# Performance work log

Hardware: AMD Instinct MI355X
Metric: run time of the kernel (lower is better)

The kernel has to match this reference:

```python
import jax, jax.numpy as jnp
import numpy as np
from jax import lax

INPUT_DIM = 512
OUTPUT_DIM = 256
MAX_HIDDEN = 1024
NUM_NODES = INPUT_DIM + OUTPUT_DIM + MAX_HIDDEN      # 1792
NUM_MID = OUTPUT_DIM + MAX_HIDDEN                    # 1280
BATCH = 16384


def setup_inputs() -> dict:
    key = jax.random.key(0)
    k1, k2, k3, k4, k5 = jax.random.split(key, 5)
    x = jax.random.normal(k1, (BATCH, INPUT_DIM), dtype=jnp.float32)
    weight = jax.random.normal(k2, (NUM_NODES, NUM_MID), dtype=jnp.float32) * 0.1
    bias = jax.random.normal(k3, (NUM_MID,), dtype=jnp.float32) * 0.1
    connectivity = jax.random.randint(k4, (NUM_NODES, NUM_MID), 0, 2, dtype=jnp.int32)
    node_existence = jax.random.randint(k5, (NUM_MID,), 0, 2, dtype=jnp.int32)
    node_existence = node_existence.at[-OUTPUT_DIM:].set(1)  # outputs always exist
    return {"x": x, "weight": weight, "bias": bias,
            "connectivity": connectivity, "node_existence": node_existence}


def reference(x, weight, bias, connectivity, node_existence):
    B = x.shape[0]
    eff_w = weight * connectivity.astype(weight.dtype)        # [N, M]
    exist = node_existence.astype(x.dtype)                    # [M]
    # results buffer [B, N]; slots >= INPUT_DIM+i are zero before step i,
    # so a full-length dot equals the torch sliced dot results[:, :input_dim+i] @ w[:input_dim+i, i].
    results = jnp.zeros((B, NUM_NODES), dtype=x.dtype).at[:, :INPUT_DIM].set(x)

    def step(results, inputs):
        i, w_col, b, e = inputs
        res = (jax.nn.sigmoid(results @ w_col) + b) * e       # [B]  (bias added AFTER sigmoid, as in torch)
        return results.at[:, INPUT_DIM + i].set(res), None

    results, _ = lax.scan(
        step, results,
        (jnp.arange(NUM_MID), eff_w.T, bias, exist))
    return results[:, -OUTPUT_DIM:]
```

## Files before the change

### kernel.cpp

```cpp
#include <hip/hip_runtime.h>

#define IN_DIM   512
#define OUT_DIM  256
#define N_MID    1280
#define BATCH    16384
#define NT       256
#define XPAD     520


#define EW2_ELEMS ((size_t)48 * 64 * 64 * 8)
#define EW2_BYTES (EW2_ELEMS * 2)
#define TRI_OFF   EW2_BYTES
#define TRI_BYTES ((size_t)32 * 1024 * 4)
#define HDR_OFF   (TRI_OFF + TRI_BYTES)
#define CMAP_OFF  (HDR_OFF + 32)
#define OCOL_OFF  (CMAP_OFF + N_MID * 4)
#define BIASC_OFF (OCOL_OFF + N_MID * 4)
#define BFX_OFF   (BIASC_OFF + N_MID * 4)
#define BFX_BYTES ((size_t)32 * 64 * 8 * 2)
#define WS_NEED   (BFX_OFF + BFX_BYTES)

#define NEG_LOG2E (-1.44269504088896340736f)

typedef __attribute__((ext_vector_type(8))) short  bfrag;
typedef __attribute__((ext_vector_type(4))) float  ffrag;

__device__ __forceinline__ unsigned short f2bf(float f) {
    unsigned int u = __float_as_uint(f);
    u += 0x7FFFu + ((u >> 16) & 1u);
    return (unsigned short)(u >> 16);
}

__device__ __forceinline__ float fast_exp2(float x) {
#if __has_builtin(__builtin_amdgcn_exp2f)
    return __builtin_amdgcn_exp2f(x);
#else
    float r;
    asm("v_exp_f32 %0, %1" : "=v"(r) : "v"(x));
    return r;
#endif
}

__device__ __forceinline__ float fast_rcp(float x) {
#if __has_builtin(__builtin_amdgcn_rcpf)
    return __builtin_amdgcn_rcpf(x);
#else
    float r;
    asm("v_rcp_f32 %0, %1" : "=v"(r) : "v"(x));
    return r;
#endif
}

__device__ __forceinline__ unsigned int cvt_pk_bf16(float lo, float hi) {
    unsigned int r;
    asm("v_cvt_pk_bf16_f32 %0, %1, %2" : "=v"(r) : "v"(lo), "v"(hi));
    return r;
}

__global__ void build_maps_kernel(const int* __restrict__ exist,
                                  const float* __restrict__ bias,
                                  int* __restrict__ hdr,
                                  int* __restrict__ cmap,
                                  int* __restrict__ ocol,
                                  float* __restrict__ biasc) {
    const int lane = threadIdx.x;
    int base = 0;
    for (int r = 0; r < N_MID / 64; ++r) {
        const int i = r * 64 + lane;
        const int e = exist[i];
        const unsigned long long m  = __ballot(e != 0);
        const unsigned long long lt = (lane == 0) ? 0ull : (~0ull >> (64 - lane));
        const int pos = base + __popcll(m & lt);
        if (e) {
            cmap[pos]  = i;
            ocol[pos]  = (i >= N_MID - OUT_DIM) ? (i - (N_MID - OUT_DIM)) : -1;
            biasc[pos] = bias[i];
        }
        base += __popcll(m);
    }
    for (int idx = base + lane; idx < N_MID; idx += 64) {
        cmap[idx] = 0; ocol[idx] = -1; biasc[idx] = 0.f;
    }
    if (lane == 0) {
        const int Mc = base;
        int Mpad;
        if (Mc <= 768) Mpad = 768;
        else if (Mc <= 1024) Mpad = 1024;
        else Mpad = (Mc + 127) & ~127;
        hdr[0] = Mc; hdr[1] = Mpad; hdr[2] = 0;
        hdr[3] = Mpad / 32; hdr[4] = Mpad / 16;
    }
}

__global__ __launch_bounds__(NT)
void gather_all_kernel(const float* __restrict__ w, const int* __restrict__ conn,
                       const int* __restrict__ hdr, const int* __restrict__ cmap,
                       unsigned short* __restrict__ ew2, float* __restrict__ tri,
                       unsigned short* __restrict__ bfx) {
    const int Mc = hdr[0], nch = hdr[3], tpm = hdr[4];
    const int bx = blockIdx.x;
    if (bx < 768) {
        if (tpm > 64) return;
        const int tid  = bx * NT + threadIdx.x;
        const int lane = tid & 63;
        const int gl   = tid >> 6;
        const int gt   = gl % tpm;
        const int kstep = gl / tpm;
        if (kstep >= 16 + nch) return;
        const int c  = gt * 16 + (lane & 15);
        const int k0 = kstep * 32 + ((lane >> 4) << 3);
        unsigned short v[8];
#pragma unroll
        for (int jj = 0; jj < 8; ++jj) {
            const int s = k0 + jj;
            float val = 0.f;
            if (c < Mc) {
                const int cc = cmap[c];
                if (s < IN_DIM) {
                    const size_t o = (size_t)s * N_MID + cc;
                    val = w[o] * (float)conn[o] * NEG_LOG2E;
                } else {
                    const int s2 = s - IN_DIM;
                    if (s2 < Mc && s2 < c && (s2 >> 5) != (c >> 5)) {
                        const size_t o = (size_t)(IN_DIM + cmap[s2]) * N_MID + cc;
                        val = w[o] * (float)conn[o] * NEG_LOG2E;
                    }
                }
            }
            v[jj] = f2bf(val);
        }
        *(uint4*)&ew2[((size_t)(kstep * tpm + gt) * 64 + lane) * 8] = *(uint4*)v;
    } else if (bx < 896) {
        if (tpm > 64) return;
        const int idx = (bx - 768) * NT + threadIdx.x;
        const int j  = idx >> 10;
        if (j >= nch) return;
        const int sl = (idx >> 5) & 31;
        const int cl = idx & 31;
        const int s = j * 32 + sl, c = j * 32 + cl;
        float v = 0.f;
        if (sl < cl && c < Mc) {
            const size_t o = (size_t)(IN_DIM + cmap[s]) * N_MID + cmap[c];
            v = w[o] * (float)conn[o] * NEG_LOG2E;
        }
        tri[idx] = v;
    } else {
        if (tpm > 64) return;
        const int j = (bx - 896) * 4 + (threadIdx.x >> 6);
        if (j >= nch || j >= 32) return;
        const int lane = threadIdx.x & 63;
        const int cl = lane & 15, qq = lane >> 4;
        const int cg = 32 * j + 16 + cl;
        unsigned short v[8];
#pragma unroll
        for (int jj = 0; jj < 8; ++jj) {
            const int k = qq * 8 + jj;
            float val = 0.f;
            if (k < 16 && cg < Mc) {
                const size_t o = (size_t)(IN_DIM + cmap[32 * j + k]) * N_MID + cmap[cg];
                val = w[o] * (float)conn[o] * NEG_LOG2E;
            }
            v[jj] = f2bf(val);
        }
        *(uint4*)&bfx[((size_t)j * 64 + lane) * 8] = *(uint4*)v;
    }
}

__device__ __forceinline__ float f4c(const float4& v, int k) {
    return (k == 0) ? v.x : (k == 1) ? v.y : (k == 2) ? v.z : v.w;
}

template <int TPW>
__global__ __launch_bounds__(256)
__attribute__((amdgpu_waves_per_eu(1, 1)))
void net7_kernel(const float* __restrict__ x,
                 const unsigned short* __restrict__ ew2,
                 const float* __restrict__ tri_g,
                 const int* __restrict__ hdr,
                 const int* __restrict__ ocol,
                 const float* __restrict__ biasc,
                 const unsigned short* __restrict__ bfx,
                 float* __restrict__ out) {
    if (hdr[1] != TPW * 64) return;
    const int Mc  = hdr[0];
    const int tpm = TPW * 4;
    const int nch = TPW * 2;

    __shared__ __align__(16) unsigned short xa[4096 * 8];
    __shared__ __align__(16) float stage2[32 * 68];
    __shared__ __align__(16) unsigned short res2[2][2048];
    __shared__ __align__(16) float tri_lds[2][1024];
    __shared__ float bias_lds[1024];
    __shared__ int   ocol_lds[1024];

    const int t = threadIdx.x, lane = t & 63, w = t >> 6;
    const int l15 = lane & 15, q = lane >> 4;
    const int r0 = blockIdx.x * 64;
    const int g0 = w * TPW;

    for (int i = t; i < TPW * 64; i += 256) {
        bias_lds[i] = biasc[i];
        ocol_lds[i] = ocol[i];
    }
    {
        uint4 z; z.x = 0u; z.y = 0u; z.z = 0u; z.w = 0u;
        uint4* r2 = (uint4*)res2;
        for (int i = t; i < 512; i += 256) r2[i] = z;
    }
    if (w == 3) {
        const float4* src = (const float4*)tri_g;
#pragma unroll
        for (int u = 0; u < 4; ++u)
            *(float4*)&tri_lds[0][(lane + 64 * u) * 4] = src[lane + 64 * u];
    }
    for (int i = t; i < 4096; i += 256) {
        const int lane2 = i & 63, rrkb = i >> 6;
        const int rr = rrkb & 3, kb = rrkb >> 2;
        const int qq = lane2 >> 4, ll = lane2 & 15;
        const int row = rr * 16 + ll;
        const int k0 = kb * 32 + qq * 8;
        const float4 f0 = *(const float4*)&x[(size_t)(r0 + row) * IN_DIM + k0];
        const float4 f1 = *(const float4*)&x[(size_t)(r0 + row) * IN_DIM + k0 + 4];
        unsigned int uu[4] = {cvt_pk_bf16(f0.x, f0.y), cvt_pk_bf16(f0.z, f0.w),
                              cvt_pk_bf16(f1.x, f1.y), cvt_pk_bf16(f1.z, f1.w)};
        *(uint4*)&xa[(size_t)i * 8] = *(uint4*)uu;
    }
    __syncthreads();

    ffrag acc[TPW][4];
#pragma unroll
    for (int tt = 0; tt < TPW; ++tt)
#pragma unroll
        for (int rr = 0; rr < 4; ++rr) acc[tt][rr] = (ffrag)0.f;

#pragma unroll 1
    for (int kb = 0; kb < 16; ++kb) {
        bfrag a[4];
#pragma unroll
        for (int rr = 0; rr < 4; ++rr)
            a[rr] = *(const bfrag*)&xa[((kb * 4 + rr) * 64 + lane) * 8];
#pragma unroll
        for (int tt = 0; tt < TPW; ++tt) {
            if ((g0 + tt) * 16 < Mc) {
                const bfrag b = *(const bfrag*)&ew2[((size_t)(kb * tpm + g0 + tt) * 64 + lane) * 8];
#pragma unroll
                for (int rr = 0; rr < 4; ++rr)
                    acc[tt][rr] = __builtin_amdgcn_mfma_f32_16x16x32_bf16(a[rr], b, acc[tt][rr], 0, 0, 0);
            }
        }
    }

    bfrag bpre[TPW];
#pragma unroll 1
    for (int j = 0; j < nch; ++j) {
        const int cbase = 32 * j;
        if (cbase >= Mc) break;

        const bfrag bc = *(const bfrag*)&bfx[((size_t)j * 64 + lane) * 8];

        if (j > 0) {
            const int pr = (j - 1) & 1;
            bfrag a[4];
#pragma unroll
            for (int rr = 0; rr < 4; ++rr)
                a[rr] = *(const bfrag*)&res2[pr][(rr * 64 + lane) * 8];
#pragma unroll
            for (int tt = 0; tt < TPW; ++tt) {
                const int col0 = (g0 + tt) * 16;
                if (col0 >= cbase && col0 < Mc) {
#pragma unroll
                    for (int rr = 0; rr < 4; ++rr)
                        acc[tt][rr] = __builtin_amdgcn_mfma_f32_16x16x32_bf16(a[rr], bpre[tt], acc[tt][rr], 0, 0, 0);
                }
            }
        }
#pragma unroll
        for (int tt = 0; tt < TPW; ++tt) {
            const int col0 = (g0 + tt) * 16;
            if (col0 >= 32 * (j + 1) && col0 < Mc)
                bpre[tt] = *(const bfrag*)&ew2[((size_t)((16 + j) * tpm + g0 + tt) * 64 + lane) * 8];
        }

        const int ow = (2 * j) / TPW;
        if (w == ow) {
#pragma unroll
            for (int tt = 0; tt < TPW; ++tt) {
                if (g0 + tt == 2 * j) {
#pragma unroll
                    for (int rr = 0; rr < 4; ++rr)
                        *(ffrag*)&stage2[l15 * 68 + rr * 16 + 4 * q] = acc[tt][rr];
                }
            }
            const float* trij = tri_lds[j & 1];
            float reg[32];
#pragma unroll
            for (int c = 0; c < 16; ++c) reg[c] = stage2[c * 68 + lane];

            float4 tr[2][8];
#pragma unroll
            for (int u = 0; u < 4; ++u) tr[0][u] = *(const float4*)&trij[u * 4];

#pragma unroll
            for (int c = 0; c < 16; ++c) {
                const int cb = c & 1;
                if (c < 15) {
#pragma unroll
                    for (int u = (c + 2) >> 2; u < 4; ++u)
                        tr[cb ^ 1][u] = *(const float4*)&trij[(c + 1) * 32 + u * 4];
                }
                const float e  = fast_exp2(reg[c]);
                const float s  = fast_rcp(1.f + e);
                const float rs = s + bias_lds[cbase + c];
                reg[c] = rs;
#pragma unroll
                for (int k = c + 1; k < 16; ++k)
                    reg[k] = fmaf(rs, f4c(tr[cb][k >> 2], k & 3), reg[k]);
            }
            unsigned short* resb = res2[j & 1];
            const int rowA = (q * 64 + l15) * 8;
#pragma unroll
            for (int qA = 0; qA < 2; ++qA) {
                unsigned int u[4];
#pragma unroll
                for (int i = 0; i < 4; ++i)
                    u[i] = cvt_pk_bf16(reg[qA * 8 + 2 * i], reg[qA * 8 + 2 * i + 1]);
                *(uint4*)&resb[rowA + qA * 128] = *(uint4*)u;
            }
            bfrag aB[4];
#pragma unroll
            for (int rr = 0; rr < 4; ++rr)
                aB[rr] = *(const bfrag*)&resb[(rr * 64 + lane) * 8];
#pragma unroll
            for (int tt = 0; tt < TPW; ++tt) {
                if (g0 + tt == 2 * j + 1) {
#pragma unroll
                    for (int rr = 0; rr < 4; ++rr)
                        acc[tt][rr] = __builtin_amdgcn_mfma_f32_16x16x32_bf16(aB[rr], bc, acc[tt][rr], 0, 0, 0);
#pragma unroll
                    for (int rr = 0; rr < 4; ++rr)
                        *(ffrag*)&stage2[(16 + l15) * 68 + rr * 16 + 4 * q] = acc[tt][rr];
                }
            }
#pragma unroll
            for (int c = 16; c < 32; ++c) reg[c] = stage2[c * 68 + lane];
#pragma unroll
            for (int u = 4; u < 8; ++u) tr[0][u] = *(const float4*)&trij[16 * 32 + u * 4];

#pragma unroll
            for (int c = 16; c < 32; ++c) {
                const int cb = c & 1;
                if (c < 31) {
#pragma unroll
                    for (int u = (c + 2) >> 2; u < 8; ++u)
                        tr[cb ^ 1][u] = *(const float4*)&trij[(c + 1) * 32 + u * 4];
                }
                const float e  = fast_exp2(reg[c]);
                const float s  = fast_rcp(1.f + e);
                const float rs = s + bias_lds[cbase + c];
                reg[c] = rs;
#pragma unroll
                for (int k = c + 1; k < 32; ++k)
                    reg[k] = fmaf(rs, f4c(tr[cb][k >> 2], k & 3), reg[k]);
            }
#pragma unroll
            for (int qA = 2; qA < 4; ++qA) {
                unsigned int u[4];
#pragma unroll
                for (int i = 0; i < 4; ++i)
                    u[i] = cvt_pk_bf16(reg[qA * 8 + 2 * i], reg[qA * 8 + 2 * i + 1]);
                *(uint4*)&resb[rowA + qA * 128] = *(uint4*)u;
            }
#pragma unroll
            for (int c4 = 0; c4 < 8; ++c4) {
                const int oc0 = ocol_lds[cbase + c4 * 4];
                const int oc3 = ocol_lds[cbase + c4 * 4 + 3];
                if (oc0 >= 0 && oc3 == oc0 + 3 && (oc0 & 3) == 0) {
                    const float4 v = make_float4(reg[c4 * 4], reg[c4 * 4 + 1],
                                                 reg[c4 * 4 + 2], reg[c4 * 4 + 3]);
                    *(float4*)&out[(size_t)(r0 + lane) * OUT_DIM + oc0] = v;
                } else {
#pragma unroll
                    for (int c = c4 * 4; c < c4 * 4 + 4; ++c) {
                        const int oc = ocol_lds[cbase + c];
                        if (oc >= 0)
                            out[(size_t)(r0 + lane) * OUT_DIM + oc] = reg[c];
                    }
                }
            }
        } else if (w == ((ow + 2) & 3)) {
            const int jn = j + 1;
            if (jn < nch && 32 * jn < Mc) {
                const float4* src = (const float4*)(tri_g + (size_t)jn * 1024);
#pragma unroll
                for (int u = 0; u < 4; ++u)
                    *(float4*)&tri_lds[jn & 1][(lane + 64 * u) * 4] = src[lane + 64 * u];
            }
        }
        __syncthreads();
    }
}

__global__ __launch_bounds__(NT, 4)
void net_v1_kernel(const float* __restrict__ x,
                   const float* __restrict__ wsrc,
                   const int* __restrict__ conn,
                   const float* __restrict__ bias,
                   const int* __restrict__ exist,
                   const int* __restrict__ hdr,
                   float* __restrict__ out) {
    if (hdr && hdr[1] <= 1024) return;
    __shared__ float xs[16 * XPAD];
    __shared__ float res_s[2][16];
    float* bias_s  = xs;
    float* exist_s = xs + N_MID;
    const int t = threadIdx.x, rg = t & 3, cg = t >> 2;
    const int r0 = blockIdx.x * 16;
    const int c0 = cg * 20;
    {
        const float4* xg = (const float4*)(x + (size_t)r0 * IN_DIM);
        for (int idx = t; idx < 16 * IN_DIM / 4; idx += NT) {
            const int r = idx >> 7, jj = idx & 127;
            *(float4*)&xs[r * XPAD + jj * 4] = xg[idx];
        }
    }
    __syncthreads();
    float acc[4][20];
#pragma unroll
    for (int a = 0; a < 4; ++a)
#pragma unroll
        for (int k = 0; k < 20; ++k) acc[a][k] = 0.f;
    for (int j = 0; j < IN_DIM; ++j) {
        const size_t woff = (size_t)j * N_MID + c0;
        const float xv0 = xs[rg * XPAD + j];
        const float xv1 = xs[(rg + 4) * XPAD + j];
        const float xv2 = xs[(rg + 8) * XPAD + j];
        const float xv3 = xs[(rg + 12) * XPAD + j];
#pragma unroll
        for (int qq = 0; qq < 5; ++qq) {
            float4 w4 = *(const float4*)(wsrc + woff + qq * 4);
            const int4 c4 = *(const int4*)(conn + woff + qq * 4);
            w4.x *= (float)c4.x; w4.y *= (float)c4.y;
            w4.z *= (float)c4.z; w4.w *= (float)c4.w;
            const float wq[4] = {w4.x, w4.y, w4.z, w4.w};
#pragma unroll
            for (int u = 0; u < 4; ++u) {
                const int k = qq * 4 + u;
                acc[0][k] = fmaf(xv0, wq[u], acc[0][k]);
                acc[1][k] = fmaf(xv1, wq[u], acc[1][k]);
                acc[2][k] = fmaf(xv2, wq[u], acc[2][k]);
                acc[3][k] = fmaf(xv3, wq[u], acc[3][k]);
            }
        }
    }
    __syncthreads();
    for (int idx = t; idx < N_MID; idx += NT) {
        bias_s[idx]  = bias[idx];
        exist_s[idx] = (float)exist[idx];
    }
    __syncthreads();
    int p = 0;
    for (int bb = 0; bb < 64; ++bb) {
#pragma unroll
        for (int kk = 0; kk < 20; ++kk) {
            const int i = bb * 20 + kk;
            const float e = exist_s[i];
            if (e != 0.f) {
                if (cg == bb) {
                    const float bv = bias_s[i];
#pragma unroll
                    for (int a = 0; a < 4; ++a) {
                        const float v = acc[a][kk];
                        const float s = __fdividef(1.f, 1.f + __expf(-v));
                        const float res = (s + bv) * e;
                        res_s[p][rg + 4 * a] = res;
                        if (i >= N_MID - OUT_DIM)
                            out[(size_t)(r0 + rg + 4 * a) * OUT_DIM + (i - (N_MID - OUT_DIM))] = res;
                    }
                }
                __syncthreads();
                const float rv0 = res_s[p][rg];
                const float rv1 = res_s[p][rg + 4];
                const float rv2 = res_s[p][rg + 8];
                const float rv3 = res_s[p][rg + 12];
                const size_t woff = (size_t)(IN_DIM + i) * N_MID + c0;
                if (cg > bb) {
#pragma unroll
                    for (int qq = 0; qq < 5; ++qq) {
                        float4 w4 = *(const float4*)(wsrc + woff + qq * 4);
                        const int4 c4 = *(const int4*)(conn + woff + qq * 4);
                        w4.x *= (float)c4.x; w4.y *= (float)c4.y;
                        w4.z *= (float)c4.z; w4.w *= (float)c4.w;
                        const float wq[4] = {w4.x, w4.y, w4.z, w4.w};
#pragma unroll
                        for (int u = 0; u < 4; ++u) {
                            const int k = qq * 4 + u;
                            acc[0][k] = fmaf(rv0, wq[u], acc[0][k]);
                            acc[1][k] = fmaf(rv1, wq[u], acc[1][k]);
                            acc[2][k] = fmaf(rv2, wq[u], acc[2][k]);
                            acc[3][k] = fmaf(rv3, wq[u], acc[3][k]);
                        }
                    }
                } else if (cg == bb) {
#pragma unroll
                    for (int k = kk + 1; k < 20; ++k) {
                        float ww = wsrc[woff + k] * (float)conn[woff + k];
                        acc[0][k] = fmaf(rv0, ww, acc[0][k]);
                        acc[1][k] = fmaf(rv1, ww, acc[1][k]);
                        acc[2][k] = fmaf(rv2, ww, acc[2][k]);
                        acc[3][k] = fmaf(rv3, ww, acc[3][k]);
                    }
                }
                p ^= 1;
            }
        }
    }
}

extern "C" void kernel_launch(void* const* d_in, const int* in_sizes, int n_in,
                              void* d_out, int out_size, void* d_ws, size_t ws_size,
                              hipStream_t stream) {
    const float* x      = (const float*)d_in[0];
    const float* weight = (const float*)d_in[1];
    const float* bias   = (const float*)d_in[2];
    const int*   conn   = (const int*)d_in[3];
    const int*   exist  = (const int*)d_in[4];
    float*       out    = (float*)d_out;

    if (ws_size >= WS_NEED) {
        char* ws = (char*)d_ws;
        unsigned short* ew2  = (unsigned short*)ws;
        float*          tri  = (float*)(ws + TRI_OFF);
        int*            hdr  = (int*)(ws + HDR_OFF);
        int*            cmap = (int*)(ws + CMAP_OFF);
        int*            ocolp= (int*)(ws + OCOL_OFF);
        float*          bsc  = (float*)(ws + BIASC_OFF);
        unsigned short* bfx  = (unsigned short*)(ws + BFX_OFF);

        build_maps_kernel<<<1, 64, 0, stream>>>(exist, bias, hdr, cmap, ocolp, bsc);
        gather_all_kernel<<<904, NT, 0, stream>>>(weight, conn, hdr, cmap, ew2, tri, bfx);
        net7_kernel<12><<<256, 256, 0, stream>>>(x, ew2, tri, hdr, ocolp, bsc, bfx, out);
        net7_kernel<16><<<256, 256, 0, stream>>>(x, ew2, tri, hdr, ocolp, bsc, bfx, out);
        net_v1_kernel<<<BATCH / 16, NT, 0, stream>>>(x, weight, conn, bias, exist, hdr, out);
    } else {
        net_v1_kernel<<<BATCH / 16, NT, 0, stream>>>(x, weight, conn, bias, exist, nullptr, out);
    }
}
```

Before: 285.1 us.

## Fold bias into precomputed column offsets and deepen triangular weight prefetch

Precomputes, per compacted column, the weighted sum of all earlier biases (cb) in a new gather branch. The serial sigmoid recurrence can then carry plain sigmoid values, with bias added only when writing outputs. This removes a dependent bias add from each step of the critical chain. The triangular weight loads also move to a 4-deep register prefetch ring instead of the previous 2-slot ping-pong. In exchange, the new cb branch runs a serial loop of up to ~1K strided global loads per thread, which may lengthen the gather kernel. Rounding also shifts slightly because bf16 now stores values without the bias.

After: 519.3 us. 82.1% more time.

```diff
diff --git a/kernel.cpp b/kernel.cpp
--- a/kernel.cpp
+++ b/kernel.cpp
@@ -18,7 +18,9 @@
 #define BIASC_OFF (OCOL_OFF + N_MID * 4)
 #define BFX_OFF   (BIASC_OFF + N_MID * 4)
 #define BFX_BYTES ((size_t)32 * 64 * 8 * 2)
-#define WS_NEED   (BFX_OFF + BFX_BYTES)
+#define CB_OFF    (BFX_OFF + BFX_BYTES)
+#define CB_BYTES  (1024 * 4)
+#define WS_NEED   (CB_OFF + CB_BYTES)
 
 #define NEG_LOG2E (-1.44269504088896340736f)
 
@@ -95,8 +97,9 @@
 __global__ __launch_bounds__(NT)
 void gather_all_kernel(const float* __restrict__ w, const int* __restrict__ conn,
                        const int* __restrict__ hdr, const int* __restrict__ cmap,
+                       const float* __restrict__ biasc,
                        unsigned short* __restrict__ ew2, float* __restrict__ tri,
-                       unsigned short* __restrict__ bfx) {
+                       unsigned short* __restrict__ bfx, float* __restrict__ cb) {
     const int Mc = hdr[0], nch = hdr[3], tpm = hdr[4];
     const int bx = blockIdx.x;
     if (bx < 768) {
@@ -144,7 +147,7 @@
             v = w[o] * (float)conn[o] * NEG_LOG2E;
         }
         tri[idx] = v;
-    } else {
+    } else if (bx < 904) {
         if (tpm > 64) return;
         const int j = (bx - 896) * 4 + (threadIdx.x >> 6);
         if (j >= nch || j >= 32) return;
@@ -163,6 +166,18 @@
             v[jj] = f2bf(val);
         }
         *(uint4*)&bfx[((size_t)j * 64 + lane) * 8] = *(uint4*)v;
+    } else {
+        if (tpm > 64) return;
+        const int k = (bx - 904) * NT + threadIdx.x;
+        float acc = 0.f;
+        if (k < Mc) {
+            const int ck = cmap[k];
+            for (int c = 0; c < k; ++c) {
+                const size_t o = (size_t)(IN_DIM + cmap[c]) * N_MID + ck;
+                acc += w[o] * (float)conn[o] * biasc[c];
+            }
+        }
+        cb[k] = acc * NEG_LOG2E;
     }
 }
 
@@ -180,6 +195,7 @@
                  const int* __restrict__ ocol,
                  const float* __restrict__ biasc,
                  const unsigned short* __restrict__ bfx,
+                 const float* __restrict__ cbg,
                  float* __restrict__ out) {
     if (hdr[1] != TPW * 64) return;
     const int Mc  = hdr[0];
@@ -191,6 +207,7 @@
     __shared__ __align__(16) unsigned short res2[2][2048];
     __shared__ __align__(16) float tri_lds[2][1024];
     __shared__ float bias_lds[1024];
+    __shared__ float cb_lds[1024];
     __shared__ int   ocol_lds[1024];
 
     const int t = threadIdx.x, lane = t & 63, w = t >> 6;
@@ -200,6 +217,7 @@
 
     for (int i = t; i < TPW * 64; i += 256) {
         bias_lds[i] = biasc[i];
+        cb_lds[i]   = cbg[i];
         ocol_lds[i] = ocol[i];
     }
     {
@@ -292,29 +310,33 @@
                 }
             }
             const float* trij = tri_lds[j & 1];
+
+            float4 tr[4][4];
+#pragma unroll
+            for (int r = 0; r < 4; ++r)
+#pragma unroll
+                for (int u = (r + 1) >> 2; u < 4; ++u)
+                    tr[r & 3][u] = *(const float4*)&trij[r * 32 + u * 4];
+
             float reg[32];
 #pragma unroll
-            for (int c = 0; c < 16; ++c) reg[c] = stage2[c * 68 + lane];
-
-            float4 tr[2][8];
-#pragma unroll
-            for (int u = 0; u < 4; ++u) tr[0][u] = *(const float4*)&trij[u * 4];
+            for (int c = 0; c < 16; ++c)
+                reg[c] = stage2[c * 68 + lane] + cb_lds[cbase + c];
 
 #pragma unroll
             for (int c = 0; c < 16; ++c) {
-                const int cb = c & 1;
-                if (c < 15) {
-#pragma unroll
-                    for (int u = (c + 2) >> 2; u < 4; ++u)
-                        tr[cb ^ 1][u] = *(const float4*)&trij[(c + 1) * 32 + u * 4];
-                }
-                const float e  = fast_exp2(reg[c]);
-                const float s  = fast_rcp(1.f + e);
-                const float rs = s + bias_lds[cbase + c];
-                reg[c] = rs;
+                const float e = fast_exp2(reg[c]);
+                const float s = fast_rcp(1.f + e);
+                reg[c] = s;
 #pragma unroll
                 for (int k = c + 1; k < 16; ++k)
-                    reg[k] = fmaf(rs, f4c(tr[cb][k >> 2], k & 3), reg[k]);
+                    reg[k] = fmaf(s, f4c(tr[c & 3][k >> 2], k & 3), reg[k]);
+                const int pf = c + 4;
+                if (pf < 15) {
+#pragma unroll
+                    for (int u = (pf + 1) >> 2; u < 4; ++u)
+                        tr[pf & 3][u] = *(const float4*)&trij[pf * 32 + u * 4];
+                }
             }
             unsigned short* resb = res2[j & 1];
             const int rowA = (q * 64 + l15) * 8;
@@ -326,6 +348,12 @@
                     u[i] = cvt_pk_bf16(reg[qA * 8 + 2 * i], reg[qA * 8 + 2 * i + 1]);
                 *(uint4*)&resb[rowA + qA * 128] = *(uint4*)u;
             }
+#pragma unroll
+            for (int r = 16; r < 20; ++r)
+#pragma unroll
+                for (int u = (r + 1) >> 2; u < 8; ++u)
+                    tr[r & 3][u - 4] = *(const float4*)&trij[r * 32 + u * 4];
+
             bfrag aB[4];
 #pragma unroll
             for (int rr = 0; rr < 4; ++rr)
@@ -342,25 +370,23 @@
                 }
             }
 #pragma unroll
-            for (int c = 16; c < 32; ++c) reg[c] = stage2[c * 68 + lane];
-#pragma unroll
-            for (int u = 4; u < 8; ++u) tr[0][u] = *(const float4*)&trij[16 * 32 + u * 4];
+            for (int c = 16; c < 32; ++c)
+                reg[c] = stage2[c * 68 + lane] + cb_lds[cbase + c];
 
 #pragma unroll
             for (int c = 16; c < 32; ++c) {
-                const int cb = c & 1;
-                if (c < 31) {
-#pragma unroll
-                    for (int u = (c + 2) >> 2; u < 8; ++u)
-                        tr[cb ^ 1][u] = *(const float4*)&trij[(c + 1) * 32 + u * 4];
-                }
-                const float e  = fast_exp2(reg[c]);
-                const float s  = fast_rcp(1.f + e);
-                const float rs = s + bias_lds[cbase + c];
-                reg[c] = rs;
+                const float e = fast_exp2(reg[c]);
+                const float s = fast_rcp(1.f + e);
+                reg[c] = s;
 #pragma unroll
                 for (int k = c + 1; k < 32; ++k)
-                    reg[k] = fmaf(rs, f4c(tr[cb][k >> 2], k & 3), reg[k]);
+                    reg[k] = fmaf(s, f4c(tr[c & 3][(k >> 2) - 4], k & 3), reg[k]);
+                const int pf = c + 4;
+                if (pf < 31) {
+#pragma unroll
+                    for (int u = (pf + 1) >> 2; u < 8; ++u)
+                        tr[pf & 3][u - 4] = *(const float4*)&trij[pf * 32 + u * 4];
+                }
             }
 #pragma unroll
             for (int qA = 2; qA < 4; ++qA) {
@@ -375,15 +401,19 @@
                 const int oc0 = ocol_lds[cbase + c4 * 4];
                 const int oc3 = ocol_lds[cbase + c4 * 4 + 3];
                 if (oc0 >= 0 && oc3 == oc0 + 3 && (oc0 & 3) == 0) {
-                    const float4 v = make_float4(reg[c4 * 4], reg[c4 * 4 + 1],
-                                                 reg[c4 * 4 + 2], reg[c4 * 4 + 3]);
+                    const float4 v = make_float4(
+                        reg[c4 * 4]     + bias_lds[cbase + c4 * 4],
+                        reg[c4 * 4 + 1] + bias_lds[cbase + c4 * 4 + 1],
+                        reg[c4 * 4 + 2] + bias_lds[cbase + c4 * 4 + 2],
+                        reg[c4 * 4 + 3] + bias_lds[cbase + c4 * 4 + 3]);
                     *(float4*)&out[(size_t)(r0 + lane) * OUT_DIM + oc0] = v;
                 } else {
 #pragma unroll
                     for (int c = c4 * 4; c < c4 * 4 + 4; ++c) {
                         const int oc = ocol_lds[cbase + c];
                         if (oc >= 0)
-                            out[(size_t)(r0 + lane) * OUT_DIM + oc] = reg[c];
+                            out[(size_t)(r0 + lane) * OUT_DIM + oc] =
+                                reg[c] + bias_lds[cbase + c];
                     }
                 }
             }
@@ -535,11 +565,13 @@
         int*            ocolp= (int*)(ws + OCOL_OFF);
         float*          bsc  = (float*)(ws + BIASC_OFF);
         unsigned short* bfx  = (unsigned short*)(ws + BFX_OFF);
+        float*          cb   = (float*)(ws + CB_OFF);
 
         build_maps_kernel<<<1, 64, 0, stream>>>(exist, bias, hdr, cmap, ocolp, bsc);
-        gather_all_kernel<<<904, NT, 0, stream>>>(weight, conn, hdr, cmap, ew2, tri, bfx);
-        net7_kernel<12><<<256, 256, 0, stream>>>(x, ew2, tri, hdr, ocolp, bsc, bfx, out);
-        net7_kernel<16><<<256, 256, 0, stream>>>(x, ew2, tri, hdr, ocolp, bsc, bfx, out);
+        gather_all_kernel<<<908, NT, 0, stream>>>(weight, conn, hdr, cmap, bsc,
+                                                  ew2, tri, bfx, cb);
+        net7_kernel<12><<<256, 256, 0, stream>>>(x, ew2, tri, hdr, ocolp, bsc, bfx, cb, out);
+        net7_kernel<16><<<256, 256, 0, stream>>>(x, ew2, tri, hdr, ocolp, bsc, bfx, cb, out);
         net_v1_kernel<<<BATCH / 16, NT, 0, stream>>>(x, weight, conn, bias, exist, hdr, out);
     } else {
         net_v1_kernel<<<BATCH / 16, NT, 0, stream>>>(x, weight, conn, bias, exist, nullptr, out);
```

## Give each wave its own 16 batch rows to remove block-wide barriers

Applied to the files above, without the earlier changes.

Rework the work split inside a block. Each of the four waves now owns 16 batch rows and all output column tiles, where before the waves split column tiles and all shared 64 rows. The serial triangular sigmoid chain therefore runs in every wave at once on its own rows, and the per-chunk __syncthreads is gone. Triangle tiles are now prefetched per wave from global into registers and then into a per-wave LDS double buffer. The cost is more B-fragment global loads per wave, since every wave reads all weight tiles, and lanes 16-63 sit idle during the packing and output steps.

Measured after the change: 615.7 us. +116.0%, slower.

```diff
diff --git a/kernel.cpp b/kernel.cpp
--- a/kernel.cpp
+++ b/kernel.cpp
@@ -173,7 +173,7 @@
 template <int TPW>
 __global__ __launch_bounds__(256)
 __attribute__((amdgpu_waves_per_eu(1, 1)))
-void net7_kernel(const float* __restrict__ x,
+void net9_kernel(const float* __restrict__ x,
                  const unsigned short* __restrict__ ew2,
                  const float* __restrict__ tri_g,
                  const int* __restrict__ hdr,
@@ -182,21 +182,21 @@
                  const unsigned short* __restrict__ bfx,
                  float* __restrict__ out) {
     if (hdr[1] != TPW * 64) return;
+    constexpr int TPM = TPW * 4;
     const int Mc  = hdr[0];
-    const int tpm = TPW * 4;
+    const int tpm = TPM;
     const int nch = TPW * 2;
 
     __shared__ __align__(16) unsigned short xa[4096 * 8];
-    __shared__ __align__(16) float stage2[32 * 68];
-    __shared__ __align__(16) unsigned short res2[2][2048];
-    __shared__ __align__(16) float tri_lds[2][1024];
+    __shared__ __align__(16) float trib_s[4][2][1024];
+    __shared__ __align__(16) float stage_s[4][32 * 20];
+    __shared__ __align__(16) unsigned short apack_s[4][512];
     __shared__ float bias_lds[1024];
     __shared__ int   ocol_lds[1024];
 
     const int t = threadIdx.x, lane = t & 63, w = t >> 6;
     const int l15 = lane & 15, q = lane >> 4;
     const int r0 = blockIdx.x * 64;
-    const int g0 = w * TPW;
 
     for (int i = t; i < TPW * 64; i += 256) {
         bias_lds[i] = biasc[i];
@@ -204,14 +204,12 @@
     }
     {
         uint4 z; z.x = 0u; z.y = 0u; z.z = 0u; z.w = 0u;
-        uint4* r2 = (uint4*)res2;
-        for (int i = t; i < 512; i += 256) r2[i] = z;
-    }
-    if (w == 3) {
-        const float4* src = (const float4*)tri_g;
-#pragma unroll
-        for (int u = 0; u < 4; ++u)
-            *(float4*)&tri_lds[0][(lane + 64 * u) * 4] = src[lane + 64 * u];
+        *(uint4*)&apack_s[w][lane * 8] = z;
+#pragma unroll
+        for (int u = 0; u < 4; ++u) {
+            const float4 tv = *(const float4*)&tri_g[u * 256 + lane * 4];
+            *(float4*)&trib_s[w][0][u * 256 + lane * 4] = tv;
+        }
     }
     for (int i = t; i < 4096; i += 256) {
         const int lane2 = i & 63, rrkb = i >> 6;
@@ -227,149 +225,132 @@
     }
     __syncthreads();
 
-    ffrag acc[TPW][4];
-#pragma unroll
-    for (int tt = 0; tt < TPW; ++tt)
-#pragma unroll
-        for (int rr = 0; rr < 4; ++rr) acc[tt][rr] = (ffrag)0.f;
+    ffrag acc[TPM];
+#pragma unroll
+    for (int tt = 0; tt < TPM; ++tt) acc[tt] = (ffrag)0.f;
 
 #pragma unroll 1
     for (int kb = 0; kb < 16; ++kb) {
-        bfrag a[4];
-#pragma unroll
-        for (int rr = 0; rr < 4; ++rr)
-            a[rr] = *(const bfrag*)&xa[((kb * 4 + rr) * 64 + lane) * 8];
-#pragma unroll
-        for (int tt = 0; tt < TPW; ++tt) {
-            if ((g0 + tt) * 16 < Mc) {
-                const bfrag b = *(const bfrag*)&ew2[((size_t)(kb * tpm + g0 + tt) * 64 + lane) * 8];
-#pragma unroll
-                for (int rr = 0; rr < 4; ++rr)
-                    acc[tt][rr] = __builtin_amdgcn_mfma_f32_16x16x32_bf16(a[rr], b, acc[tt][rr], 0, 0, 0);
-            }
-        }
-    }
-
-    bfrag bpre[TPW];
+        const bfrag a = *(const bfrag*)&xa[((kb * 4 + w) * 64 + lane) * 8];
+#pragma unroll
+        for (int tt = 0; tt < TPM; ++tt) {
+            if (tt * 16 < Mc) {
+                const bfrag b = *(const bfrag*)&ew2[((size_t)(kb * tpm + tt) * 64 + lane) * 8];
+                acc[tt] = __builtin_amdgcn_mfma_f32_16x16x32_bf16(a, b, acc[tt], 0, 0, 0);
+            }
+        }
+    }
+
+    float* stg = stage_s[w];
+    unsigned short* apk = apack_s[w];
+    const int wrow0 = r0 + 16 * w;
+
 #pragma unroll 1
     for (int j = 0; j < nch; ++j) {
         const int cbase = 32 * j;
         if (cbase >= Mc) break;
 
+        const bool tok = (j + 1 < nch) && (32 * (j + 1) < Mc);
+        float4 tpre[4];
+        if (tok) {
+#pragma unroll
+            for (int u = 0; u < 4; ++u)
+                tpre[u] = *(const float4*)&tri_g[(size_t)(j + 1) * 1024 + u * 256 + lane * 4];
+        }
         const bfrag bc = *(const bfrag*)&bfx[((size_t)j * 64 + lane) * 8];
 
-        if (j > 0) {
-            const int pr = (j - 1) & 1;
-            bfrag a[4];
-#pragma unroll
-            for (int rr = 0; rr < 4; ++rr)
-                a[rr] = *(const bfrag*)&res2[pr][(rr * 64 + lane) * 8];
-#pragma unroll
-            for (int tt = 0; tt < TPW; ++tt) {
-                const int col0 = (g0 + tt) * 16;
-                if (col0 >= cbase && col0 < Mc) {
-#pragma unroll
-                    for (int rr = 0; rr < 4; ++rr)
-                        acc[tt][rr] = __builtin_amdgcn_mfma_f32_16x16x32_bf16(a[rr], bpre[tt], acc[tt][rr], 0, 0, 0);
-                }
-            }
-        }
-#pragma unroll
-        for (int tt = 0; tt < TPW; ++tt) {
-            const int col0 = (g0 + tt) * 16;
-            if (col0 >= 32 * (j + 1) && col0 < Mc)
-                bpre[tt] = *(const bfrag*)&ew2[((size_t)((16 + j) * tpm + g0 + tt) * 64 + lane) * 8];
-        }
-
-        const int ow = (2 * j) / TPW;
-        if (w == ow) {
-#pragma unroll
-            for (int tt = 0; tt < TPW; ++tt) {
-                if (g0 + tt == 2 * j) {
-#pragma unroll
-                    for (int rr = 0; rr < 4; ++rr)
-                        *(ffrag*)&stage2[l15 * 68 + rr * 16 + 4 * q] = acc[tt][rr];
-                }
-            }
-            const float* trij = tri_lds[j & 1];
-            float reg[32];
-#pragma unroll
-            for (int c = 0; c < 16; ++c) reg[c] = stage2[c * 68 + lane];
-
-            float4 tr[2][8];
-#pragma unroll
-            for (int u = 0; u < 4; ++u) tr[0][u] = *(const float4*)&trij[u * 4];
-
-#pragma unroll
-            for (int c = 0; c < 16; ++c) {
-                const int cb = c & 1;
-                if (c < 15) {
-#pragma unroll
-                    for (int u = (c + 2) >> 2; u < 4; ++u)
-                        tr[cb ^ 1][u] = *(const float4*)&trij[(c + 1) * 32 + u * 4];
-                }
-                const float e  = fast_exp2(reg[c]);
-                const float s  = fast_rcp(1.f + e);
-                const float rs = s + bias_lds[cbase + c];
-                reg[c] = rs;
-#pragma unroll
-                for (int k = c + 1; k < 16; ++k)
-                    reg[k] = fmaf(rs, f4c(tr[cb][k >> 2], k & 3), reg[k]);
-            }
-            unsigned short* resb = res2[j & 1];
-            const int rowA = (q * 64 + l15) * 8;
+#pragma unroll
+        for (int tt = 0; tt < TPM; ++tt)
+            if (tt == 2 * j)
+                *(ffrag*)&stg[l15 * 20 + 4 * q] = acc[tt];
+
+        const float* trij = &trib_s[w][j & 1][0];
+        float reg[32];
+#pragma unroll
+        for (int c = 0; c < 16; ++c) reg[c] = stg[c * 20 + l15];
+
+        float4 tr[2][8];
+#pragma unroll
+        for (int u = 0; u < 4; ++u) tr[0][u] = *(const float4*)&trij[u * 4];
+
+#pragma unroll
+        for (int c = 0; c < 16; ++c) {
+            const int cb = c & 1;
+            if (c < 15) {
+#pragma unroll
+                for (int u = (c + 2) >> 2; u < 4; ++u)
+                    tr[cb ^ 1][u] = *(const float4*)&trij[(c + 1) * 32 + u * 4];
+            }
+            const float e  = fast_exp2(reg[c]);
+            const float s  = fast_rcp(1.f + e);
+            const float rs = s + bias_lds[cbase + c];
+            reg[c] = rs;
+#pragma unroll
+            for (int k = c + 1; k < 16; ++k)
+                reg[k] = fmaf(rs, f4c(tr[cb][k >> 2], k & 3), reg[k]);
+        }
+        if (lane < 16) {
 #pragma unroll
             for (int qA = 0; qA < 2; ++qA) {
                 unsigned int u[4];
 #pragma unroll
                 for (int i = 0; i < 4; ++i)
                     u[i] = cvt_pk_bf16(reg[qA * 8 + 2 * i], reg[qA * 8 + 2 * i + 1]);
-                *(uint4*)&resb[rowA + qA * 128] = *(uint4*)u;
-            }
-            bfrag aB[4];
-#pragma unroll
-            for (int rr = 0; rr < 4; ++rr)
-                aB[rr] = *(const bfrag*)&resb[(rr * 64 + lane) * 8];
-#pragma unroll
-            for (int tt = 0; tt < TPW; ++tt) {
-                if (g0 + tt == 2 * j + 1) {
-#pragma unroll
-                    for (int rr = 0; rr < 4; ++rr)
-                        acc[tt][rr] = __builtin_amdgcn_mfma_f32_16x16x32_bf16(aB[rr], bc, acc[tt][rr], 0, 0, 0);
-#pragma unroll
-                    for (int rr = 0; rr < 4; ++rr)
-                        *(ffrag*)&stage2[(16 + l15) * 68 + rr * 16 + 4 * q] = acc[tt][rr];
+                *(uint4*)&apk[lane * 32 + qA * 8] = *(uint4*)u;
+            }
+        }
+        {
+            const bfrag aB = *(const bfrag*)&apk[l15 * 32 + q * 8];
+#pragma unroll
+            for (int tt = 0; tt < TPM; ++tt) {
+                if (tt == 2 * j + 1) {
+                    acc[tt] = __builtin_amdgcn_mfma_f32_16x16x32_bf16(aB, bc, acc[tt], 0, 0, 0);
+                    *(ffrag*)&stg[(16 + l15) * 20 + 4 * q] = acc[tt];
                 }
             }
-#pragma unroll
-            for (int c = 16; c < 32; ++c) reg[c] = stage2[c * 68 + lane];
-#pragma unroll
-            for (int u = 4; u < 8; ++u) tr[0][u] = *(const float4*)&trij[16 * 32 + u * 4];
-
-#pragma unroll
-            for (int c = 16; c < 32; ++c) {
-                const int cb = c & 1;
-                if (c < 31) {
-#pragma unroll
-                    for (int u = (c + 2) >> 2; u < 8; ++u)
-                        tr[cb ^ 1][u] = *(const float4*)&trij[(c + 1) * 32 + u * 4];
-                }
-                const float e  = fast_exp2(reg[c]);
-                const float s  = fast_rcp(1.f + e);
-                const float rs = s + bias_lds[cbase + c];
-                reg[c] = rs;
-#pragma unroll
-                for (int k = c + 1; k < 32; ++k)
-                    reg[k] = fmaf(rs, f4c(tr[cb][k >> 2], k & 3), reg[k]);
-            }
+        }
+#pragma unroll
+        for (int c = 16; c < 32; ++c) reg[c] = stg[c * 20 + l15];
+#pragma unroll
+        for (int u = 4; u < 8; ++u) tr[0][u] = *(const float4*)&trij[16 * 32 + u * 4];
+
+#pragma unroll
+        for (int c = 16; c < 32; ++c) {
+            const int cb = c & 1;
+            if (c < 31) {
+#pragma unroll
+                for (int u = (c + 2) >> 2; u < 8; ++u)
+                    tr[cb ^ 1][u] = *(const float4*)&trij[(c + 1) * 32 + u * 4];
+            }
+            const float e  = fast_exp2(reg[c]);
+            const float s  = fast_rcp(1.f + e);
+            const float rs = s + bias_lds[cbase + c];
+            reg[c] = rs;
+#pragma unroll
+            for (int k = c + 1; k < 32; ++k)
+                reg[k] = fmaf(rs, f4c(tr[cb][k >> 2], k & 3), reg[k]);
+        }
+        if (lane < 16) {
 #pragma unroll
             for (int qA = 2; qA < 4; ++qA) {
                 unsigned int u[4];
 #pragma unroll
                 for (int i = 0; i < 4; ++i)
                     u[i] = cvt_pk_bf16(reg[qA * 8 + 2 * i], reg[qA * 8 + 2 * i + 1]);
-                *(uint4*)&resb[rowA + qA * 128] = *(uint4*)u;
-            }
+                *(uint4*)&apk[lane * 32 + qA * 8] = *(uint4*)u;
+            }
+        }
+        {
+            const bfrag aF = *(const bfrag*)&apk[l15 * 32 + q * 8];
+#pragma unroll
+            for (int tt = 0; tt < TPM; ++tt) {
+                if (tt >= 2 * j + 2 && tt * 16 < Mc) {
+                    const bfrag b = *(const bfrag*)&ew2[((size_t)((16 + j) * tpm + tt) * 64 + lane) * 8];
+                    acc[tt] = __builtin_amdgcn_mfma_f32_16x16x32_bf16(aF, b, acc[tt], 0, 0, 0);
+                }
+            }
+        }
+        if (lane < 16) {
 #pragma unroll
             for (int c4 = 0; c4 < 8; ++c4) {
                 const int oc0 = ocol_lds[cbase + c4 * 4];
@@ -377,26 +358,22 @@
                 if (oc0 >= 0 && oc3 == oc0 + 3 && (oc0 & 3) == 0) {
                     const float4 v = make_float4(reg[c4 * 4], reg[c4 * 4 + 1],
                                                  reg[c4 * 4 + 2], reg[c4 * 4 + 3]);
-                    *(float4*)&out[(size_t)(r0 + lane) * OUT_DIM + oc0] = v;
+                    *(float4*)&out[(size_t)(wrow0 + lane) * OUT_DIM + oc0] = v;
                 } else {
 #pragma unroll
                     for (int c = c4 * 4; c < c4 * 4 + 4; ++c) {
                         const int oc = ocol_lds[cbase + c];
                         if (oc >= 0)
-                            out[(size_t)(r0 + lane) * OUT_DIM + oc] = reg[c];
+                            out[(size_t)(wrow0 + lane) * OUT_DIM + oc] = reg[c];
                     }
                 }
             }
-        } else if (w == ((ow + 2) & 3)) {
-            const int jn = j + 1;
-            if (jn < nch && 32 * jn < Mc) {
-                const float4* src = (const float4*)(tri_g + (size_t)jn * 1024);
-#pragma unroll
-                for (int u = 0; u < 4; ++u)
-                    *(float4*)&tri_lds[jn & 1][(lane + 64 * u) * 4] = src[lane + 64 * u];
-            }
-        }
-        __syncthreads();
+        }
+        if (tok) {
+#pragma unroll
+            for (int u = 0; u < 4; ++u)
+                *(float4*)&trib_s[w][(j + 1) & 1][u * 256 + lane * 4] = tpre[u];
+        }
     }
 }
 
@@ -538,8 +515,8 @@
 
         build_maps_kernel<<<1, 64, 0, stream>>>(exist, bias, hdr, cmap, ocolp, bsc);
         gather_all_kernel<<<904, NT, 0, stream>>>(weight, conn, hdr, cmap, ew2, tri, bfx);
-        net7_kernel<12><<<256, 256, 0, stream>>>(x, ew2, tri, hdr, ocolp, bsc, bfx, out);
-        net7_kernel<16><<<256, 256, 0, stream>>>(x, ew2, tri, hdr, ocolp, bsc, bfx, out);
+        net9_kernel<12><<<BATCH / 64, 256, 0, stream>>>(x, ew2, tri, hdr, ocolp, bsc, bfx, out);
+        net9_kernel<16><<<BATCH / 64, 256, 0, stream>>>(x, ew2, tri, hdr, ocolp, bsc, bfx, out);
         net_v1_kernel<<<BATCH / 16, NT, 0, stream>>>(x, weight, conn, bias, exist, hdr, out);
     } else {
         net_v1_kernel<<<BATCH / 16, NT, 0, stream>>>(x, weight, conn, bias, exist, nullptr, out);
```

## Add per-wave pipelined net10 kernel for the 12-tile recurrence path

Applied to the files above, without the earlier changes.

Adds a new recurrence kernel for the TPW=12 configuration. Each wave keeps private LDS history and triangle buffers and no block-wide barriers run inside the column loop. Each 32-column chunk is processed as two 16-column halves so the sigmoid recurrence of the first half can overlap the MFMA for the second half. The next chunk's triangular coefficients are prefetched into a double buffer. This adds LDS usage and code complexity, and it relies on the node-count header matching the 12-tile configuration.

Result: slower. 338.8 us (+18.8%).

```diff
diff --git a/kernel.cpp b/kernel.cpp
--- a/kernel.cpp
+++ b/kernel.cpp
@@ -168,6 +168,203 @@
 
 __device__ __forceinline__ float f4c(const float4& v, int k) {
     return (k == 0) ? v.x : (k == 1) ? v.y : (k == 2) ? v.z : v.w;
+}
+
+template <int TPW>
+__global__ __launch_bounds__(256)
+__attribute__((amdgpu_waves_per_eu(1, 1)))
+void net10_kernel(const float* __restrict__ x,
+                  const unsigned short* __restrict__ ew2,
+                  const float* __restrict__ tri_g,
+                  const int* __restrict__ hdr,
+                  const int* __restrict__ ocol,
+                  const float* __restrict__ biasc,
+                  const unsigned short* __restrict__ bfx,
+                  float* __restrict__ out) {
+    if (hdr[1] != TPW * 64) return;
+    constexpr int TPM = TPW * 4;
+    constexpr int NCH = TPW * 2;
+    const int Mc = hdr[0];
+
+    __shared__ __align__(16) unsigned short hist_s[4][NCH * 512];
+    __shared__ __align__(16) float trib_s[4][2][1024];
+    __shared__ __align__(16) float stage_s[4][32 * 20];
+    __shared__ float bias_lds[TPW * 64];
+    __shared__ int   ocol_lds[TPW * 64];
+
+    const int t = threadIdx.x, lane = t & 63, w = t >> 6;
+    const int l15 = lane & 15, q = lane >> 4;
+    const int r0 = blockIdx.x * 64;
+    const int wrow0 = r0 + 16 * w;
+
+    for (int i = t; i < TPW * 64; i += 256) {
+        bias_lds[i] = biasc[i];
+        ocol_lds[i] = ocol[i];
+    }
+    {
+        uint4 z; z.x = 0u; z.y = 0u; z.z = 0u; z.w = 0u;
+        uint4* h4 = (uint4*)hist_s[w];
+        for (int i = lane; i < NCH * 64; i += 64) h4[i] = z;
+#pragma unroll
+        for (int u = 0; u < 4; ++u)
+            *(float4*)&trib_s[w][0][u * 256 + lane * 4] =
+                *(const float4*)&tri_g[u * 256 + lane * 4];
+    }
+    bfrag xf[16];
+#pragma unroll
+    for (int kb = 0; kb < 16; ++kb) {
+        const float4 f0 = *(const float4*)&x[(size_t)(wrow0 + l15) * IN_DIM + kb * 32 + q * 8];
+        const float4 f1 = *(const float4*)&x[(size_t)(wrow0 + l15) * IN_DIM + kb * 32 + q * 8 + 4];
+        unsigned int uu[4] = {cvt_pk_bf16(f0.x, f0.y), cvt_pk_bf16(f0.z, f0.w),
+                              cvt_pk_bf16(f1.x, f1.y), cvt_pk_bf16(f1.z, f1.w)};
+        xf[kb] = *(const bfrag*)uu;
+    }
+    __syncthreads();
+
+    unsigned short* hist = hist_s[w];
+    float* stg = stage_s[w];
+
+#pragma unroll 1
+    for (int j = 0; j < NCH; ++j) {
+        const int cbase = 32 * j;
+        if (cbase >= Mc) break;
+        const int t0 = 2 * j, t1 = 2 * j + 1;
+
+        const bool tok = (j + 1 < NCH) && (32 * (j + 1) < Mc);
+        float4 tpre[4];
+        if (tok) {
+#pragma unroll
+            for (int u = 0; u < 4; ++u)
+                tpre[u] = *(const float4*)&tri_g[(size_t)(j + 1) * 1024 + u * 256 + lane * 4];
+        }
+        const bfrag bc = *(const bfrag*)&bfx[((size_t)j * 64 + lane) * 8];
+
+        ffrag acc0 = (ffrag)0.f, acc1 = (ffrag)0.f;
+#pragma unroll
+        for (int kb = 0; kb < 16; ++kb) {
+            const bfrag b0 = *(const bfrag*)&ew2[((size_t)(kb * TPM + t0) * 64 + lane) * 8];
+            const bfrag b1 = *(const bfrag*)&ew2[((size_t)(kb * TPM + t1) * 64 + lane) * 8];
+            acc0 = __builtin_amdgcn_mfma_f32_16x16x32_bf16(xf[kb], b0, acc0, 0, 0, 0);
+            acc1 = __builtin_amdgcn_mfma_f32_16x16x32_bf16(xf[kb], b1, acc1, 0, 0, 0);
+        }
+        {
+            bfrag af = {}, b0 = {}, b1 = {};
+            if (j > 0) {
+                af = *(const bfrag*)&hist[lane * 8];
+                b0 = *(const bfrag*)&ew2[((size_t)(16 * TPM + t0) * 64 + lane) * 8];
+                b1 = *(const bfrag*)&ew2[((size_t)(16 * TPM + t1) * 64 + lane) * 8];
+            }
+#pragma unroll 2
+            for (int p = 0; p < j; ++p) {
+                bfrag afn = af, bn0 = b0, bn1 = b1;
+                if (p + 1 < j) {
+                    afn = *(const bfrag*)&hist[(size_t)(p + 1) * 512 + lane * 8];
+                    bn0 = *(const bfrag*)&ew2[((size_t)((17 + p) * TPM + t0) * 64 + lane) * 8];
+                    bn1 = *(const bfrag*)&ew2[((size_t)((17 + p) * TPM + t1) * 64 + lane) * 8];
+                }
+                acc0 = __builtin_amdgcn_mfma_f32_16x16x32_bf16(af, b0, acc0, 0, 0, 0);
+                acc1 = __builtin_amdgcn_mfma_f32_16x16x32_bf16(af, b1, acc1, 0, 0, 0);
+                af = afn; b0 = bn0; b1 = bn1;
+            }
+        }
+
+        *(ffrag*)&stg[l15 * 20 + 4 * q] = acc0;
+
+        const float* trij = &trib_s[w][j & 1][0];
+        float reg[32];
+#pragma unroll
+        for (int c = 0; c < 16; ++c) reg[c] = stg[c * 20 + l15];
+
+        float4 tr[2][8];
+#pragma unroll
+        for (int u = 0; u < 4; ++u) tr[0][u] = *(const float4*)&trij[u * 4];
+
+#pragma unroll
+        for (int c = 0; c < 16; ++c) {
+            const int cb = c & 1;
+            if (c < 15) {
+#pragma unroll
+                for (int u = (c + 2) >> 2; u < 4; ++u)
+                    tr[cb ^ 1][u] = *(const float4*)&trij[(c + 1) * 32 + u * 4];
+            }
+            const float e  = fast_exp2(reg[c]);
+            const float s  = fast_rcp(1.f + e);
+            const float rs = s + bias_lds[cbase + c];
+            reg[c] = rs;
+#pragma unroll
+            for (int k = c + 1; k < 16; ++k)
+                reg[k] = fmaf(rs, f4c(tr[cb][k >> 2], k & 3), reg[k]);
+        }
+        unsigned short* hj = &hist[(size_t)j * 512];
+        if (lane < 16) {
+#pragma unroll
+            for (int qA = 0; qA < 2; ++qA) {
+                unsigned int u[4];
+#pragma unroll
+                for (int i = 0; i < 4; ++i)
+                    u[i] = cvt_pk_bf16(reg[qA * 8 + 2 * i], reg[qA * 8 + 2 * i + 1]);
+                *(uint4*)&hj[(size_t)(qA * 16 + lane) * 8] = *(uint4*)u;
+            }
+        }
+        {
+            const bfrag aB = *(const bfrag*)&hj[lane * 8];
+            acc1 = __builtin_amdgcn_mfma_f32_16x16x32_bf16(aB, bc, acc1, 0, 0, 0);
+            *(ffrag*)&stg[(16 + l15) * 20 + 4 * q] = acc1;
+        }
+#pragma unroll
+        for (int c = 16; c < 32; ++c) reg[c] = stg[c * 20 + l15];
+#pragma unroll
+        for (int u = 4; u < 8; ++u) tr[0][u] = *(const float4*)&trij[16 * 32 + u * 4];
+
+#pragma unroll
+        for (int c = 16; c < 32; ++c) {
+            const int cb = c & 1;
+            if (c < 31) {
+#pragma unroll
+                for (int u = (c + 2) >> 2; u < 8; ++u)
+                    tr[cb ^ 1][u] = *(const float4*)&trij[(c + 1) * 32 + u * 4];
+            }
+            const float e  = fast_exp2(reg[c]);
+            const float s  = fast_rcp(1.f + e);
+            const float rs = s + bias_lds[cbase + c];
+            reg[c] = rs;
+#pragma unroll
+            for (int k = c + 1; k < 32; ++k)
+                reg[k] = fmaf(rs, f4c(tr[cb][k >> 2], k & 3), reg[k]);
+        }
+        if (lane < 16) {
+#pragma unroll
+            for (int qA = 2; qA < 4; ++qA) {
+                unsigned int u[4];
+#pragma unroll
+                for (int i = 0; i < 4; ++i)
+                    u[i] = cvt_pk_bf16(reg[qA * 8 + 2 * i], reg[qA * 8 + 2 * i + 1]);
+                *(uint4*)&hj[(size_t)(qA * 16 + lane) * 8] = *(uint4*)u;
+            }
+#pragma unroll
+            for (int c4 = 0; c4 < 8; ++c4) {
+                const int oc0 = ocol_lds[cbase + c4 * 4];
+                const int oc3 = ocol_lds[cbase + c4 * 4 + 3];
+                if (oc0 >= 0 && oc3 == oc0 + 3 && (oc0 & 3) == 0) {
+                    const float4 v = make_float4(reg[c4 * 4], reg[c4 * 4 + 1],
+                                                 reg[c4 * 4 + 2], reg[c4 * 4 + 3]);
+                    *(float4*)&out[(size_t)(wrow0 + lane) * OUT_DIM + oc0] = v;
+                } else {
+#pragma unroll
+                    for (int c = c4 * 4; c < c4 * 4 + 4; ++c) {
+                        const int oc = ocol_lds[cbase + c];
+                        if (oc >= 0)
+                            out[(size_t)(wrow0 + lane) * OUT_DIM + oc] = reg[c];
+                    }
+                }
+            }
+        }
+        if (tok) {
+#pragma unroll
+            for (int u = 0; u < 4; ++u)
+                *(float4*)&trib_s[w][(j + 1) & 1][u * 256 + lane * 4] = tpre[u];
+        }
+    }
 }
 
 template <int TPW>
@@ -538,8 +735,8 @@
 
         build_maps_kernel<<<1, 64, 0, stream>>>(exist, bias, hdr, cmap, ocolp, bsc);
         gather_all_kernel<<<904, NT, 0, stream>>>(weight, conn, hdr, cmap, ew2, tri, bfx);
-        net7_kernel<12><<<256, 256, 0, stream>>>(x, ew2, tri, hdr, ocolp, bsc, bfx, out);
-        net7_kernel<16><<<256, 256, 0, stream>>>(x, ew2, tri, hdr, ocolp, bsc, bfx, out);
+        net10_kernel<12><<<BATCH / 64, 256, 0, stream>>>(x, ew2, tri, hdr, ocolp, bsc, bfx, out);
+        net7_kernel<16><<<BATCH / 64, 256, 0, stream>>>(x, ew2, tri, hdr, ocolp, bsc, bfx, out);
         net_v1_kernel<<<BATCH / 16, NT, 0, stream>>>(x, weight, conn, bias, exist, hdr, out);
     } else {
         net_v1_kernel<<<BATCH / 16, NT, 0, stream>>>(x, weight, conn, bias, exist, nullptr, out);
```
